# Kernel optimization log

Measured on AMD Instinct MI355X. Metric: run time of the kernel, lower is better.

The kernel has to match this reference:

```python
import jax, jax.numpy as jnp
import numpy as np

N = 50000       # nodes
E = 800000      # edges (avg degree 16)
IN = 256        # input feature dim
HID = 64        # per-head hidden dim
H = 2           # heads
C = 64          # num_classes (final single-head layer width)
NEG_SLOPE = 0.01  # torch F.leaky_relu default


def setup_inputs() -> dict:
    key = jax.random.key(0)
    ks = jax.random.split(key, 24)
    nrm = lambda k, shape, scale: jax.random.normal(k, shape, jnp.float32) * scale
    features = nrm(ks[0], (N, IN), 1.0)
    src = jax.random.randint(ks[1], (E,), 0, N)
    dst = jax.random.randint(ks[2], (E,), 0, N)
    # layer 0: H heads, Linear(IN->HID) + attn_l/attn_r Linear(HID->1)
    W0 = nrm(ks[3], (H, IN, HID), IN ** -0.5)
    b0 = jnp.zeros((H, HID), jnp.float32)
    al0 = nrm(ks[4], (H, HID), HID ** -0.5)
    bl0 = jnp.zeros((H,), jnp.float32)
    ar0 = nrm(ks[5], (H, HID), HID ** -0.5)
    br0 = jnp.zeros((H,), jnp.float32)
    # layer 1: H heads, Linear(H*HID->HID)
    W1 = nrm(ks[6], (H, H * HID, HID), (H * HID) ** -0.5)
    b1 = jnp.zeros((H, HID), jnp.float32)
    al1 = nrm(ks[7], (H, HID), HID ** -0.5)
    bl1 = jnp.zeros((H,), jnp.float32)
    ar1 = nrm(ks[8], (H, HID), HID ** -0.5)
    br1 = jnp.zeros((H,), jnp.float32)
    # final: 1 head, Linear(H*HID->C)
    Wf = nrm(ks[9], (1, H * HID, C), (H * HID) ** -0.5)
    bf = jnp.zeros((1, C), jnp.float32)
    alf = nrm(ks[10], (1, C), C ** -0.5)
    blf = jnp.zeros((1,), jnp.float32)
    arf = nrm(ks[11], (1, C), C ** -0.5)
    brf = jnp.zeros((1,), jnp.float32)
    return dict(features=features, src=src, dst=dst,
                W0=W0, b0=b0, al0=al0, bl0=bl0, ar0=ar0, br0=br0,
                W1=W1, b1=b1, al1=al1, bl1=bl1, ar1=ar1, br1=br1,
                Wf=Wf, bf=bf, alf=alf, blf=blf, arf=arf, brf=brf)


def gat_layer(x, src, dst, W, b, al, bl, ar, br):
    # x: [N, D]; W: [H, D, K]
    ft = jnp.einsum('nd,hdk->nhk', x, W) + b          # [N,H,K]
    a1 = jnp.einsum('nhk,hk->nh', ft, al) + bl        # [N,H] (dst-side)
    a2 = jnp.einsum('nhk,hk->nh', ft, ar) + br        # [N,H] (src-side)
    s = jax.nn.leaky_relu(a1[dst] + a2[src], NEG_SLOPE)  # [E,H]
    m = jax.ops.segment_max(s, dst, num_segments=N)      # per-dst max for stable softmax
    e = jnp.exp(s - m[dst])
    denom = jax.ops.segment_sum(e, dst, num_segments=N)
    alpha = e / denom[dst]                               # edge softmax over in-neighbors
    accum = jax.ops.segment_sum(alpha[:, :, None] * ft[src], dst, num_segments=N)  # [N,H,K]
    return jax.nn.elu(accum)


def reference(features, src, dst,
              W0, b0, al0, bl0, ar0, br0,
              W1, b1, al1, bl1, ar1, br1,
              Wf, bf, alf, blf, arf, brf):
    x = gat_layer(features, src, dst, W0, b0, al0, bl0, ar0, br0).reshape(N, H * HID)
    x = gat_layer(x, src, dst, W1, b1, al1, bl1, ar1, br1).reshape(N, H * HID)
    out = gat_layer(x, src, dst, Wf, bf, alf, blf, arf, brf)[:, 0, :]  # [N,C]
    return out
```

## Files before the change

kernel.cpp:

```cpp
#include <hip/hip_runtime.h>
#include <math.h>

#define NN 50000
#define EE 800000
#define DIN 256
#define NEG_SLOPE 0.01f

typedef __attribute__((ext_vector_type(8))) short bf16x8;
typedef __attribute__((ext_vector_type(8))) unsigned short u16x8;
typedef __attribute__((ext_vector_type(4))) float f32x4;
typedef __attribute__((ext_vector_type(2))) _Float16 f16x2;

__device__ __forceinline__ unsigned short bf16_rne(float f) {
    unsigned int u = __float_as_uint(f);
    u += 0x7fffu + ((u >> 16) & 1u);
    return (unsigned short)(u >> 16);
}
__device__ __forceinline__ float bf16_tof(unsigned short h) {
    return __uint_as_float(((unsigned int)h) << 16);
}

__global__ __launch_bounds__(256) void histrank_kernel(const int* __restrict__ dst,
                                                       int* __restrict__ cnt,
                                                       int* __restrict__ pos, int E) {
    int e = blockIdx.x * 256 + threadIdx.x;
    if (e < E) pos[e] = atomicAdd(&cnt[dst[e]], 1);
}

__global__ __launch_bounds__(1024) void scanA_kernel(const int* __restrict__ cnt,
                                                     int* __restrict__ off,
                                                     int* __restrict__ aux, int Nn) {
    __shared__ int wsums[16];
    int tid = threadIdx.x, lane = tid & 63, w = tid >> 6;
    int i = blockIdx.x * 1024 + tid;
    int v = (i < Nn) ? cnt[i] : 0;
    int x = v;
#pragma unroll
    for (int d = 1; d < 64; d <<= 1) {
        int y = __shfl_up(x, d);
        if (lane >= d) x += y;
    }
    if (lane == 63) wsums[w] = x;
    __syncthreads();
    if (w == 0 && lane < 16) {
        int ws = wsums[lane];
#pragma unroll
        for (int d = 1; d < 16; d <<= 1) {
            int y = __shfl_up(ws, d);
            if (lane >= d) ws += y;
        }
        wsums[lane] = ws;
    }
    __syncthreads();
    int incl = x + (w > 0 ? wsums[w - 1] : 0);
    if (i < Nn) off[i + 1] = incl;
    if (tid == 1023) aux[blockIdx.x] = incl;
}

__global__ __launch_bounds__(1024) void scanC_kernel(const int* __restrict__ aux,
                                                     int* __restrict__ off, int Nn) {
    int b = blockIdx.x;
    int prefix = 0;
    for (int j = 0; j < b; j++) prefix += aux[j];
    int i = b * 1024 + threadIdx.x;
    if (i < Nn) off[i + 1] += prefix;
    if (i == 0 && b == 0) off[0] = 0;
}

__global__ __launch_bounds__(256) void scatter_kernel(const int* __restrict__ src,
                                                      const int* __restrict__ dst,
                                                      const int* __restrict__ off,
                                                      const int* __restrict__ pos,
                                                      int* __restrict__ esrc, int E) {
    int e = blockIdx.x * 256 + threadIdx.x;
    if (e >= E) return;
    int d = dst[e];
    esrc[off[d] + pos[e]] = src[e];
}

__global__ __launch_bounds__(256) void conv_w_kernel(
    const float* __restrict__ W0, const float* __restrict__ W1,
    const float* __restrict__ Wf, unsigned short* __restrict__ w0h,
    unsigned short* __restrict__ w0l, unsigned short* __restrict__ w1h,
    unsigned short* __restrict__ w1l, unsigned short* __restrict__ wfh,
    unsigned short* __restrict__ wfl) {
    int t = blockIdx.x * 256 + threadIdx.x;
    const float* W;
    unsigned short *oh, *ol;
    int D, u;
    if (t < 32768) { W = W0; oh = w0h; ol = w0l; D = 256; u = t; }
    else if (t < 49152) { W = W1; oh = w1h; ol = w1l; D = 128; u = t - 32768; }
    else if (t < 57344) { W = Wf; oh = wfh; ol = wfl; D = 128; u = t - 49152; }
    else return;
    int d = u & (D - 1);
    int n = u / D;
    float v = W[((size_t)(n >> 6) * D + d) * 64 + (n & 63)];
    unsigned short hi = bf16_rne(v);
    unsigned short lo = bf16_rne(v - bf16_tof(hi));
    oh[(size_t)n * D + d] = hi;
    ol[(size_t)n * D + d] = lo;
}

#define LDK 40

template <int NCOL, bool AFP32>
__global__ __launch_bounds__(256) void gemm_attn(
    const float* __restrict__ Xf, const unsigned short* __restrict__ Xhi,
    const unsigned short* __restrict__ Xlo, const unsigned short* __restrict__ Wthi,
    const unsigned short* __restrict__ Wtlo, const float* __restrict__ bias,
    const float* __restrict__ al, const float* __restrict__ bl,
    const float* __restrict__ ar, const float* __restrict__ br,
    _Float16* __restrict__ FT, float* __restrict__ A1, float* __restrict__ A2,
    int Nn, int D) {
    const int H = NCOL / 64;
    const int NC16 = NCOL / 16;
    __shared__ __align__(16) unsigned short Ahi_s[64 * LDK];
    __shared__ __align__(16) unsigned short Alo_s[64 * LDK];
    __shared__ __align__(16) unsigned short Bhi_s[NCOL * LDK];
    __shared__ __align__(16) unsigned short Blo_s[NCOL * LDK];

    int tid = threadIdx.x;
    int wv = tid >> 6, l = tid & 63, lm = l & 15, quad = l >> 4;
    int m0 = blockIdx.x * 64;

    f32x4 acc[NC16];
#pragma unroll
    for (int c = 0; c < NC16; c++) acc[c] = (f32x4){0.f, 0.f, 0.f, 0.f};

    for (int d0 = 0; d0 < D; d0 += 32) {
        if (AFP32) {
#pragma unroll
            for (int i = 0; i < 2; i++) {
                int u = tid + i * 256;
                int row = u >> 3, c4 = u & 7;
                float4 v = make_float4(0.f, 0.f, 0.f, 0.f);
                if (m0 + row < Nn)
                    v = *(const float4*)&Xf[(size_t)(m0 + row) * D + d0 + c4 * 4];
                float f[4] = {v.x, v.y, v.z, v.w};
                unsigned short hi[4], lo[4];
#pragma unroll
                for (int j = 0; j < 4; j++) {
                    hi[j] = bf16_rne(f[j]);
                    lo[j] = bf16_rne(f[j] - bf16_tof(hi[j]));
                }
                *(ushort4*)&Ahi_s[row * LDK + c4 * 4] = make_ushort4(hi[0], hi[1], hi[2], hi[3]);
                *(ushort4*)&Alo_s[row * LDK + c4 * 4] = make_ushort4(lo[0], lo[1], lo[2], lo[3]);
            }
        } else {
            int row = tid >> 2, q = tid & 3;
            u16x8 vh = (u16x8)0, vl = (u16x8)0;
            if (m0 + row < Nn) {
                vh = *(const u16x8*)&Xhi[(size_t)(m0 + row) * D + d0 + q * 8];
                vl = *(const u16x8*)&Xlo[(size_t)(m0 + row) * D + d0 + q * 8];
            }
            *(u16x8*)&Ahi_s[row * LDK + q * 8] = vh;
            *(u16x8*)&Alo_s[row * LDK + q * 8] = vl;
        }
#pragma unroll
        for (int i = 0; i < NCOL / 64; i++) {
            int u = tid + i * 256;
            int n = u >> 2, q = u & 3;
            *(u16x8*)&Bhi_s[n * LDK + q * 8] =
                *(const u16x8*)&Wthi[(size_t)n * D + d0 + q * 8];
            *(u16x8*)&Blo_s[n * LDK + q * 8] =
                *(const u16x8*)&Wtlo[(size_t)n * D + d0 + q * 8];
        }
        __syncthreads();

        int arow = wv * 16 + lm;
        bf16x8 ah = *(const bf16x8*)&Ahi_s[arow * LDK + quad * 8];
        bf16x8 alo = *(const bf16x8*)&Alo_s[arow * LDK + quad * 8];
#pragma unroll
        for (int c = 0; c < NC16; c++) {
            bf16x8 bh = *(const bf16x8*)&Bhi_s[(c * 16 + lm) * LDK + quad * 8];
            bf16x8 blo = *(const bf16x8*)&Blo_s[(c * 16 + lm) * LDK + quad * 8];
            acc[c] = __builtin_amdgcn_mfma_f32_16x16x32_bf16(ah, bh, acc[c], 0, 0, 0);
            acc[c] = __builtin_amdgcn_mfma_f32_16x16x32_bf16(ah, blo, acc[c], 0, 0, 0);
            acc[c] = __builtin_amdgcn_mfma_f32_16x16x32_bf16(alo, bh, acc[c], 0, 0, 0);
        }
        __syncthreads();
    }

    float bj[NC16], alj[NC16], arj[NC16];
#pragma unroll
    for (int c = 0; c < NC16; c++) {
        bj[c] = bias[c * 16 + lm];
        alj[c] = al[c * 16 + lm];
        arj[c] = ar[c * 16 + lm];
    }
#pragma unroll
    for (int reg = 0; reg < 4; reg++) {
        int row = m0 + wv * 16 + quad * 4 + reg;
        bool ok = row < Nn;
        float s1[H], s2[H];
#pragma unroll
        for (int h = 0; h < H; h++) { s1[h] = 0.f; s2[h] = 0.f; }
#pragma unroll
        for (int c = 0; c < NC16; c++) {
            float o = acc[c][reg] + bj[c];
            int h = c >> 2;
            s1[h] += o * alj[c];
            s2[h] += o * arj[c];
            if (ok) FT[(size_t)row * NCOL + c * 16 + lm] = (_Float16)o;
        }
#pragma unroll
        for (int h = 0; h < H; h++) {
#pragma unroll
            for (int d = 1; d < 16; d <<= 1) {
                s1[h] += __shfl_xor(s1[h], d);
                s2[h] += __shfl_xor(s2[h], d);
            }
        }
        if (ok && lm == 0) {
#pragma unroll
            for (int h = 0; h < H; h++) {
                A1[(size_t)row * H + h] = s1[h] + bl[h];
                A2[(size_t)row * H + h] = s2[h] + br[h];
            }
        }
    }
}

__global__ __launch_bounds__(256) void agg2_kernel(
    const _Float16* __restrict__ ft, const float* __restrict__ a1,
    const float* __restrict__ a2, const int* __restrict__ off,
    const int* __restrict__ esrc, unsigned short* __restrict__ ohi,
    unsigned short* __restrict__ olo, int Nn) {
    __shared__ __align__(16) float ws[4][128];
    __shared__ __align__(16) int sjs[4][64];
    int wv = threadIdx.x >> 6, lane = threadIdx.x & 63;
    int n = blockIdx.x * 4 + wv;
    if (n >= Nn) return;
    int o0 = off[n], deg = off[n + 1] - o0;
    int hs = lane >> 5, cl2 = lane * 2;
    if (deg == 0) {
        *(ushort2*)&ohi[(size_t)n * 128 + cl2] = make_ushort2(0, 0);
        *(ushort2*)&olo[(size_t)n * 128 + cl2] = make_ushort2(0, 0);
        return;
    }
    float2 a1v = *(const float2*)&a1[(size_t)n * 2];
    float ax = 0.f, ay = 0.f;
    float ds0 = 0.f, ds1 = 0.f;
    for (int e0 = 0; e0 < deg; e0 += 64) {
        int nE = min(64, deg - e0);
        float w0 = 0.f, w1 = 0.f;
        int sj = 0;
        if (lane < nE) {
            sj = esrc[o0 + e0 + lane];
            float2 a2j = *(const float2*)&a2[(size_t)sj * 2];
            float t0 = a1v.x + a2j.x;
            float t1 = a1v.y + a2j.y;
            t0 = t0 > 0.f ? t0 : NEG_SLOPE * t0;
            t1 = t1 > 0.f ? t1 : NEG_SLOPE * t1;
            w0 = __expf(t0);
            w1 = __expf(t1);
        }
        ds0 += w0;
        ds1 += w1;
        *(float2*)&ws[wv][lane * 2] = make_float2(w0, w1);
        sjs[wv][lane] = sj;
        int j = 0;
        for (; j + 8 <= nE; j += 8) {
            float wb[8];
            int sb[8];
#pragma unroll
            for (int u = 0; u < 8; u++) {
                wb[u] = ws[wv][(j + u) * 2 + hs];
                sb[u] = sjs[wv][j + u];
            }
            f16x2 f[8];
#pragma unroll
            for (int u = 0; u < 8; u++)
                f[u] = *(const f16x2*)&ft[(size_t)sb[u] * 128 + cl2];
#pragma unroll
            for (int u = 0; u < 8; u++) {
                ax += wb[u] * (float)f[u].x;
                ay += wb[u] * (float)f[u].y;
            }
        }
        for (; j < nE; j++) {
            float w = ws[wv][j * 2 + hs];
            int s0 = sjs[wv][j];
            f16x2 f = *(const f16x2*)&ft[(size_t)s0 * 128 + cl2];
            ax += w * (float)f.x;
            ay += w * (float)f.y;
        }
    }
#pragma unroll
    for (int d = 1; d < 64; d <<= 1) {
        ds0 += __shfl_xor(ds0, d);
        ds1 += __shfl_xor(ds1, d);
    }
    float rd = 1.f / (hs ? ds1 : ds0);
    float rx = ax * rd, ry = ay * rd;
    rx = rx > 0.f ? rx : expm1f(rx);
    ry = ry > 0.f ? ry : expm1f(ry);
    unsigned short hx = bf16_rne(rx), hy = bf16_rne(ry);
    unsigned short lx = bf16_rne(rx - bf16_tof(hx)), ly = bf16_rne(ry - bf16_tof(hy));
    *(ushort2*)&ohi[(size_t)n * 128 + cl2] = make_ushort2(hx, hy);
    *(ushort2*)&olo[(size_t)n * 128 + cl2] = make_ushort2(lx, ly);
}

__global__ __launch_bounds__(256) void agg1_kernel(
    const _Float16* __restrict__ ft, const float* __restrict__ a1,
    const float* __restrict__ a2, const int* __restrict__ off,
    const int* __restrict__ esrc, float* __restrict__ out, int Nn) {
    __shared__ __align__(16) float ws[4][64];
    __shared__ __align__(16) int sjs[4][64];
    int wv = threadIdx.x >> 6, lane = threadIdx.x & 63;
    int n = blockIdx.x * 4 + wv;
    if (n >= Nn) return;
    int o0 = off[n], deg = off[n + 1] - o0;
    if (deg == 0) {
        out[(size_t)n * 64 + lane] = 0.f;
        return;
    }
    float a1v = a1[n];
    float acc = 0.f, dsum = 0.f;
    for (int e0 = 0; e0 < deg; e0 += 64) {
        int nE = min(64, deg - e0);
        float wl = 0.f;
        int sj = 0;
        if (lane < nE) {
            sj = esrc[o0 + e0 + lane];
            float t = a1v + a2[sj];
            t = t > 0.f ? t : NEG_SLOPE * t;
            wl = __expf(t);
        }
        dsum += wl;
        ws[wv][lane] = wl;
        sjs[wv][lane] = sj;
        int j = 0;
        for (; j + 8 <= nE; j += 8) {
            float wb[8];
            int sb[8];
#pragma unroll
            for (int u = 0; u < 8; u++) {
                wb[u] = ws[wv][j + u];
                sb[u] = sjs[wv][j + u];
            }
            _Float16 f[8];
#pragma unroll
            for (int u = 0; u < 8; u++) f[u] = ft[(size_t)sb[u] * 64 + lane];
#pragma unroll
            for (int u = 0; u < 8; u++) acc += wb[u] * (float)f[u];
        }
        for (; j < nE; j++)
            acc += ws[wv][j] * (float)ft[(size_t)sjs[wv][j] * 64 + lane];
    }
#pragma unroll
    for (int d = 1; d < 64; d <<= 1) dsum += __shfl_xor(dsum, d);
    float r = acc / dsum;
    out[(size_t)n * 64 + lane] = r > 0.f ? r : expm1f(r);
}

extern "C" void kernel_launch(void* const* d_in, const int* in_sizes, int n_in,
                              void* d_out, int out_size, void* d_ws, size_t ws_size,
                              hipStream_t stream) {
    const float* features = (const float*)d_in[0];
    const int* src = (const int*)d_in[1];
    const int* dst = (const int*)d_in[2];
    const float* W0 = (const float*)d_in[3];
    const float* b0 = (const float*)d_in[4];
    const float* al0 = (const float*)d_in[5];
    const float* bl0 = (const float*)d_in[6];
    const float* ar0 = (const float*)d_in[7];
    const float* br0 = (const float*)d_in[8];
    const float* W1 = (const float*)d_in[9];
    const float* b1 = (const float*)d_in[10];
    const float* al1 = (const float*)d_in[11];
    const float* bl1 = (const float*)d_in[12];
    const float* ar1 = (const float*)d_in[13];
    const float* br1 = (const float*)d_in[14];
    const float* Wf = (const float*)d_in[15];
    const float* bf = (const float*)d_in[16];
    const float* alf = (const float*)d_in[17];
    const float* blf = (const float*)d_in[18];
    const float* arf = (const float*)d_in[19];
    const float* brf = (const float*)d_in[20];

    char* p = (char*)d_ws;
    auto carve = [&](size_t bytes) {
        void* q = (void*)p;
        p += (bytes + 255) & ~(size_t)255;
        return q;
    };
    _Float16* ft = (_Float16*)carve((size_t)NN * 128 * 2);
    unsigned short* Xhi = (unsigned short*)carve((size_t)NN * 128 * 2);
    unsigned short* Xlo = (unsigned short*)carve((size_t)NN * 128 * 2);
    float* a1 = (float*)carve((size_t)NN * 2 * 4);
    float* a2 = (float*)carve((size_t)NN * 2 * 4);
    int* off = (int*)carve((size_t)(NN + 1) * 4);
    int* cnt = (int*)carve((size_t)NN * 4);
    int* esrc = (int*)carve((size_t)EE * 4);
    int* pos = (int*)carve((size_t)EE * 4);
    int* aux = (int*)carve(64 * 4);
    unsigned short* w0h = (unsigned short*)carve(32768 * 2);
    unsigned short* w0l = (unsigned short*)carve(32768 * 2);
    unsigned short* w1h = (unsigned short*)carve(16384 * 2);
    unsigned short* w1l = (unsigned short*)carve(16384 * 2);
    unsigned short* wfh = (unsigned short*)carve(8192 * 2);
    unsigned short* wfl = (unsigned short*)carve(8192 * 2);

    const int NB_SCAN = (NN + 1023) / 1024;
    const int GE = (EE + 255) / 256;

    hipMemsetAsync(cnt, 0, (size_t)NN * 4, stream);
    histrank_kernel<<<GE, 256, 0, stream>>>(dst, cnt, pos, EE);
    scanA_kernel<<<NB_SCAN, 1024, 0, stream>>>(cnt, off, aux, NN);
    scanC_kernel<<<NB_SCAN, 1024, 0, stream>>>(aux, off, NN);
    scatter_kernel<<<GE, 256, 0, stream>>>(src, dst, off, pos, esrc, EE);
    conv_w_kernel<<<(57344 + 255) / 256, 256, 0, stream>>>(W0, W1, Wf, w0h, w0l, w1h,
                                                           w1l, wfh, wfl);

    const int gx = (NN + 63) / 64;
    const int gn = (NN + 3) / 4;

    gemm_attn<128, true><<<gx, 256, 0, stream>>>(features, nullptr, nullptr, w0h, w0l,
                                                 b0, al0, bl0, ar0, br0, ft, a1, a2,
                                                 NN, DIN);
    agg2_kernel<<<gn, 256, 0, stream>>>(ft, a1, a2, off, esrc, Xhi, Xlo, NN);

    gemm_attn<128, false><<<gx, 256, 0, stream>>>(nullptr, Xhi, Xlo, w1h, w1l, b1, al1,
                                                  bl1, ar1, br1, ft, a1, a2, NN, 128);
    agg2_kernel<<<gn, 256, 0, stream>>>(ft, a1, a2, off, esrc, Xhi, Xlo, NN);

    gemm_attn<64, false><<<gx, 256, 0, stream>>>(nullptr, Xhi, Xlo, wfh, wfl, bf, alf,
                                                 blf, arf, brf, ft, a1, a2, NN, 128);
    agg1_kernel<<<gn, 256, 0, stream>>>(ft, a1, a2, off, esrc, (float*)d_out, NN);
}
```

Measured before the change: 339.4 us.

## Vectorize GAT aggregation gathers to 16-byte loads with cross-lane reduction

Both aggregation kernels now give each lane 8 contiguous fp16 features, read with one 16-byte load. Instead of every lane walking all edges for its own 1-2 columns, a wavefront handles several edges at once (4 edge groups in agg2, 8 in agg1), and the partial sums are combined with xor shuffles at the end. This cuts the number of gather instructions and widens each memory transaction, aiming at the gather-bound edge loop. The cost is a shuffle reduction over 8 accumulators, extra registers, and wasted work on tail edges when the degree is not a multiple of the group size.

```diff
diff --git a/kernel.cpp b/kernel.cpp
--- a/kernel.cpp
+++ b/kernel.cpp
@@ -9,7 +9,7 @@
 typedef __attribute__((ext_vector_type(8))) short bf16x8;
 typedef __attribute__((ext_vector_type(8))) unsigned short u16x8;
 typedef __attribute__((ext_vector_type(4))) float f32x4;
-typedef __attribute__((ext_vector_type(2))) _Float16 f16x2;
+typedef __attribute__((ext_vector_type(8))) _Float16 f16x8;
 
 __device__ __forceinline__ unsigned short bf16_rne(float f) {
     unsigned int u = __float_as_uint(f);
@@ -232,15 +232,21 @@
     int n = blockIdx.x * 4 + wv;
     if (n >= Nn) return;
     int o0 = off[n], deg = off[n + 1] - o0;
-    int hs = lane >> 5, cl2 = lane * 2;
+    int eg = lane >> 4, c = lane & 15, head = c >> 3;
     if (deg == 0) {
-        *(ushort2*)&ohi[(size_t)n * 128 + cl2] = make_ushort2(0, 0);
-        *(ushort2*)&olo[(size_t)n * 128 + cl2] = make_ushort2(0, 0);
+        if (lane < 16) {
+            u16x8 z = (u16x8)0;
+            *(u16x8*)&ohi[(size_t)n * 128 + c * 8] = z;
+            *(u16x8*)&olo[(size_t)n * 128 + c * 8] = z;
+        }
         return;
     }
     float2 a1v = *(const float2*)&a1[(size_t)n * 2];
-    float ax = 0.f, ay = 0.f;
+    float acc8[8];
+#pragma unroll
+    for (int k = 0; k < 8; k++) acc8[k] = 0.f;
     float ds0 = 0.f, ds1 = 0.f;
+
     for (int e0 = 0; e0 < deg; e0 += 64) {
         int nE = min(64, deg - e0);
         float w0 = 0.f, w1 = 0.f;
@@ -259,31 +265,14 @@
         ds1 += w1;
         *(float2*)&ws[wv][lane * 2] = make_float2(w0, w1);
         sjs[wv][lane] = sj;
-        int j = 0;
-        for (; j + 8 <= nE; j += 8) {
-            float wb[8];
-            int sb[8];
-#pragma unroll
-            for (int u = 0; u < 8; u++) {
-                wb[u] = ws[wv][(j + u) * 2 + hs];
-                sb[u] = sjs[wv][j + u];
-            }
-            f16x2 f[8];
-#pragma unroll
-            for (int u = 0; u < 8; u++)
-                f[u] = *(const f16x2*)&ft[(size_t)sb[u] * 128 + cl2];
-#pragma unroll
-            for (int u = 0; u < 8; u++) {
-                ax += wb[u] * (float)f[u].x;
-                ay += wb[u] * (float)f[u].y;
-            }
-        }
-        for (; j < nE; j++) {
-            float w = ws[wv][j * 2 + hs];
-            int s0 = sjs[wv][j];
-            f16x2 f = *(const f16x2*)&ft[(size_t)s0 * 128 + cl2];
-            ax += w * (float)f.x;
-            ay += w * (float)f.y;
+#pragma unroll 4
+        for (int j = 0; j < nE; j += 4) {
+            int jj = j + eg;
+            float w = (jj < nE) ? ws[wv][jj * 2 + head] : 0.f;
+            int s0 = sjs[wv][jj & 63];
+            f16x8 f = *(const f16x8*)&ft[(size_t)s0 * 128 + c * 8];
+#pragma unroll
+            for (int k = 0; k < 8; k++) acc8[k] += w * (float)f[k];
         }
     }
 #pragma unroll
@@ -291,14 +280,25 @@
         ds0 += __shfl_xor(ds0, d);
         ds1 += __shfl_xor(ds1, d);
     }
-    float rd = 1.f / (hs ? ds1 : ds0);
-    float rx = ax * rd, ry = ay * rd;
-    rx = rx > 0.f ? rx : expm1f(rx);
-    ry = ry > 0.f ? ry : expm1f(ry);
-    unsigned short hx = bf16_rne(rx), hy = bf16_rne(ry);
-    unsigned short lx = bf16_rne(rx - bf16_tof(hx)), ly = bf16_rne(ry - bf16_tof(hy));
-    *(ushort2*)&ohi[(size_t)n * 128 + cl2] = make_ushort2(hx, hy);
-    *(ushort2*)&olo[(size_t)n * 128 + cl2] = make_ushort2(lx, ly);
+#pragma unroll
+    for (int k = 0; k < 8; k++) {
+        acc8[k] += __shfl_xor(acc8[k], 16);
+        acc8[k] += __shfl_xor(acc8[k], 32);
+    }
+    if (lane < 16) {
+        float rd = 1.f / (head ? ds1 : ds0);
+        u16x8 hi8, lo8;
+#pragma unroll
+        for (int k = 0; k < 8; k++) {
+            float r = acc8[k] * rd;
+            r = r > 0.f ? r : expm1f(r);
+            unsigned short h = bf16_rne(r);
+            hi8[k] = h;
+            lo8[k] = bf16_rne(r - bf16_tof(h));
+        }
+        *(u16x8*)&ohi[(size_t)n * 128 + c * 8] = hi8;
+        *(u16x8*)&olo[(size_t)n * 128 + c * 8] = lo8;
+    }
 }
 
 __global__ __launch_bounds__(256) void agg1_kernel(
@@ -311,12 +311,19 @@
     int n = blockIdx.x * 4 + wv;
     if (n >= Nn) return;
     int o0 = off[n], deg = off[n + 1] - o0;
+    int eg = lane >> 3, c = lane & 7;
     if (deg == 0) {
-        out[(size_t)n * 64 + lane] = 0.f;
+        if (lane < 8) {
+            *(float4*)&out[(size_t)n * 64 + c * 8] = make_float4(0, 0, 0, 0);
+            *(float4*)&out[(size_t)n * 64 + c * 8 + 4] = make_float4(0, 0, 0, 0);
+        }
         return;
     }
     float a1v = a1[n];
-    float acc = 0.f, dsum = 0.f;
+    float acc8[8];
+#pragma unroll
+    for (int k = 0; k < 8; k++) acc8[k] = 0.f;
+    float dsum = 0.f;
     for (int e0 = 0; e0 < deg; e0 += 64) {
         int nE = min(64, deg - e0);
         float wl = 0.f;
@@ -330,28 +337,35 @@
         dsum += wl;
         ws[wv][lane] = wl;
         sjs[wv][lane] = sj;
-        int j = 0;
-        for (; j + 8 <= nE; j += 8) {
-            float wb[8];
-            int sb[8];
-#pragma unroll
-            for (int u = 0; u < 8; u++) {
-                wb[u] = ws[wv][j + u];
-                sb[u] = sjs[wv][j + u];
-            }
-            _Float16 f[8];
-#pragma unroll
-            for (int u = 0; u < 8; u++) f[u] = ft[(size_t)sb[u] * 64 + lane];
-#pragma unroll
-            for (int u = 0; u < 8; u++) acc += wb[u] * (float)f[u];
-        }
-        for (; j < nE; j++)
-            acc += ws[wv][j] * (float)ft[(size_t)sjs[wv][j] * 64 + lane];
+#pragma unroll 4
+        for (int j = 0; j < nE; j += 8) {
+            int jj = j + eg;
+            float w = (jj < nE) ? ws[wv][jj] : 0.f;
+            int s0 = sjs[wv][jj & 63];
+            f16x8 f = *(const f16x8*)&ft[(size_t)s0 * 64 + c * 8];
+#pragma unroll
+            for (int k = 0; k < 8; k++) acc8[k] += w * (float)f[k];
+        }
     }
 #pragma unroll
     for (int d = 1; d < 64; d <<= 1) dsum += __shfl_xor(dsum, d);
-    float r = acc / dsum;
-    out[(size_t)n * 64 + lane] = r > 0.f ? r : expm1f(r);
+#pragma unroll
+    for (int k = 0; k < 8; k++) {
+        acc8[k] += __shfl_xor(acc8[k], 8);
+        acc8[k] += __shfl_xor(acc8[k], 16);
+        acc8[k] += __shfl_xor(acc8[k], 32);
+    }
+    if (lane < 8) {
+        float rd = 1.f / dsum;
+        float r[8];
+#pragma unroll
+        for (int k = 0; k < 8; k++) {
+            r[k] = acc8[k] * rd;
+            r[k] = r[k] > 0.f ? r[k] : expm1f(r[k]);
+        }
+        *(float4*)&out[(size_t)n * 64 + c * 8] = make_float4(r[0], r[1], r[2], r[3]);
+        *(float4*)&out[(size_t)n * 64 + c * 8 + 4] = make_float4(r[4], r[5], r[6], r[7]);
+    }
 }
 
 extern "C" void kernel_launch(void* const* d_in, const int* in_sizes, int n_in,
```

Result: slower. 346.2 us (+2.0%).

## Merge preprocessing launches: fuse histogram with weight conversion, scatter with first GEMM

Applied to the files above, without the earlier changes.

Cuts the launch count by combining independent work into shared grids. The histogram/rank pass and the weight bf16 split run in one kernel. The two-pass scan becomes a single kernel where each block recomputes its prefix from the counts. The CSR scatter shares a grid with the layer-0 GEMM, so their blocks can overlap. This trades launch gaps and serialization for redundant prefix reads in later scan blocks and a larger mixed-role grid.

```diff
diff --git a/kernel.cpp b/kernel.cpp
--- a/kernel.cpp
+++ b/kernel.cpp
@@ -20,71 +20,20 @@
     return __uint_as_float(((unsigned int)h) << 16);
 }
 
-__global__ __launch_bounds__(256) void histrank_kernel(const int* __restrict__ dst,
-                                                       int* __restrict__ cnt,
-                                                       int* __restrict__ pos, int E) {
-    int e = blockIdx.x * 256 + threadIdx.x;
-    if (e < E) pos[e] = atomicAdd(&cnt[dst[e]], 1);
-}
-
-__global__ __launch_bounds__(1024) void scanA_kernel(const int* __restrict__ cnt,
-                                                     int* __restrict__ off,
-                                                     int* __restrict__ aux, int Nn) {
-    __shared__ int wsums[16];
-    int tid = threadIdx.x, lane = tid & 63, w = tid >> 6;
-    int i = blockIdx.x * 1024 + tid;
-    int v = (i < Nn) ? cnt[i] : 0;
-    int x = v;
-#pragma unroll
-    for (int d = 1; d < 64; d <<= 1) {
-        int y = __shfl_up(x, d);
-        if (lane >= d) x += y;
-    }
-    if (lane == 63) wsums[w] = x;
-    __syncthreads();
-    if (w == 0 && lane < 16) {
-        int ws = wsums[lane];
-#pragma unroll
-        for (int d = 1; d < 16; d <<= 1) {
-            int y = __shfl_up(ws, d);
-            if (lane >= d) ws += y;
-        }
-        wsums[lane] = ws;
-    }
-    __syncthreads();
-    int incl = x + (w > 0 ? wsums[w - 1] : 0);
-    if (i < Nn) off[i + 1] = incl;
-    if (tid == 1023) aux[blockIdx.x] = incl;
-}
-
-__global__ __launch_bounds__(1024) void scanC_kernel(const int* __restrict__ aux,
-                                                     int* __restrict__ off, int Nn) {
-    int b = blockIdx.x;
-    int prefix = 0;
-    for (int j = 0; j < b; j++) prefix += aux[j];
-    int i = b * 1024 + threadIdx.x;
-    if (i < Nn) off[i + 1] += prefix;
-    if (i == 0 && b == 0) off[0] = 0;
-}
-
-__global__ __launch_bounds__(256) void scatter_kernel(const int* __restrict__ src,
-                                                      const int* __restrict__ dst,
-                                                      const int* __restrict__ off,
-                                                      const int* __restrict__ pos,
-                                                      int* __restrict__ esrc, int E) {
-    int e = blockIdx.x * 256 + threadIdx.x;
-    if (e >= E) return;
-    int d = dst[e];
-    esrc[off[d] + pos[e]] = src[e];
-}
-
-__global__ __launch_bounds__(256) void conv_w_kernel(
+__global__ __launch_bounds__(256) void fused_pre(
+    const int* __restrict__ dst, int* __restrict__ cnt, int* __restrict__ pos, int E,
     const float* __restrict__ W0, const float* __restrict__ W1,
     const float* __restrict__ Wf, unsigned short* __restrict__ w0h,
     unsigned short* __restrict__ w0l, unsigned short* __restrict__ w1h,
     unsigned short* __restrict__ w1l, unsigned short* __restrict__ wfh,
-    unsigned short* __restrict__ wfl) {
-    int t = blockIdx.x * 256 + threadIdx.x;
+    unsigned short* __restrict__ wfl, int histBlocks) {
+    int b = blockIdx.x;
+    if (b < histBlocks) {
+        int e = b * 256 + threadIdx.x;
+        if (e < E) pos[e] = atomicAdd(&cnt[dst[e]], 1);
+        return;
+    }
+    int t = (b - histBlocks) * 256 + threadIdx.x;
     const float* W;
     unsigned short *oh, *ol;
     int D, u;
@@ -101,11 +50,59 @@
     ol[(size_t)n * D + d] = lo;
 }
 
+__global__ __launch_bounds__(1024) void scan_one(const int* __restrict__ cnt,
+                                                 int* __restrict__ off, int Nn) {
+    __shared__ int wsums[16];
+    __shared__ int s_prefix;
+    int tid = threadIdx.x, lane = tid & 63, w = tid >> 6;
+    int base = blockIdx.x * 1024;
+    int p = 0;
+    for (int i = tid; i < base; i += 1024) p += cnt[i];
+#pragma unroll
+    for (int d = 1; d < 64; d <<= 1) p += __shfl_xor(p, d);
+    if (tid < 16) wsums[tid] = 0;
+    __syncthreads();
+    if (lane == 0) wsums[w] = p;
+    __syncthreads();
+    if (tid == 0) {
+        int t = 0;
+#pragma unroll
+        for (int k = 0; k < 16; k++) t += wsums[k];
+        s_prefix = t;
+    }
+    __syncthreads();
+    int prefix = s_prefix;
+    __syncthreads();
+    int i = base + tid;
+    int v = (i < Nn) ? cnt[i] : 0;
+    int x = v;
+#pragma unroll
+    for (int d = 1; d < 64; d <<= 1) {
+        int y = __shfl_up(x, d);
+        if (lane >= d) x += y;
+    }
+    if (lane == 63) wsums[w] = x;
+    __syncthreads();
+    if (w == 0 && lane < 16) {
+        int ws = wsums[lane];
+#pragma unroll
+        for (int d = 1; d < 16; d <<= 1) {
+            int y = __shfl_up(ws, d);
+            if (lane >= d) ws += y;
+        }
+        wsums[lane] = ws;
+    }
+    __syncthreads();
+    int incl = x + (w > 0 ? wsums[w - 1] : 0);
+    if (i < Nn) off[i + 1] = prefix + incl;
+    if (blockIdx.x == 0 && tid == 0) off[0] = 0;
+}
+
 #define LDK 40
 
 template <int NCOL, bool AFP32>
-__global__ __launch_bounds__(256) void gemm_attn(
-    const float* __restrict__ Xf, const unsigned short* __restrict__ Xhi,
+__device__ __forceinline__ void gemm_body(
+    int bx, const float* __restrict__ Xf, const unsigned short* __restrict__ Xhi,
     const unsigned short* __restrict__ Xlo, const unsigned short* __restrict__ Wthi,
     const unsigned short* __restrict__ Wtlo, const float* __restrict__ bias,
     const float* __restrict__ al, const float* __restrict__ bl,
@@ -121,7 +118,7 @@
 
     int tid = threadIdx.x;
     int wv = tid >> 6, l = tid & 63, lm = l & 15, quad = l >> 4;
-    int m0 = blockIdx.x * 64;
+    int m0 = bx * 64;
 
     f32x4 acc[NC16];
 #pragma unroll
@@ -219,6 +216,40 @@
             }
         }
     }
+}
+
+template <int NCOL, bool AFP32>
+__global__ __launch_bounds__(256) void gemm_attn(
+    const float* __restrict__ Xf, const unsigned short* __restrict__ Xhi,
+    const unsigned short* __restrict__ Xlo, const unsigned short* __restrict__ Wthi,
+    const unsigned short* __restrict__ Wtlo, const float* __restrict__ bias,
+    const float* __restrict__ al, const float* __restrict__ bl,
+    const float* __restrict__ ar, const float* __restrict__ br,
+    _Float16* __restrict__ FT, float* __restrict__ A1, float* __restrict__ A2,
+    int Nn, int D) {
+    gemm_body<NCOL, AFP32>(blockIdx.x, Xf, Xhi, Xlo, Wthi, Wtlo, bias, al, bl, ar, br,
+                           FT, A1, A2, Nn, D);
+}
+
+__global__ __launch_bounds__(256) void fused_mid(
+    const int* __restrict__ src, const int* __restrict__ dst,
+    const int* __restrict__ off, const int* __restrict__ pos,
+    int* __restrict__ esrc, int E, const float* __restrict__ Xf,
+    const unsigned short* __restrict__ Wthi, const unsigned short* __restrict__ Wtlo,
+    const float* __restrict__ bias, const float* __restrict__ al,
+    const float* __restrict__ bl, const float* __restrict__ ar,
+    const float* __restrict__ br, _Float16* __restrict__ FT,
+    float* __restrict__ A1, float* __restrict__ A2, int Nn, int D, int scBlocks) {
+    if (blockIdx.x < scBlocks) {
+        int e = blockIdx.x * 256 + threadIdx.x;
+        if (e < E) {
+            int d = dst[e];
+            esrc[off[d] + pos[e]] = src[e];
+        }
+        return;
+    }
+    gemm_body<128, true>(blockIdx.x - scBlocks, Xf, nullptr, nullptr, Wthi, Wtlo,
+                         bias, al, bl, ar, br, FT, A1, A2, Nn, D);
 }
 
 __global__ __launch_bounds__(256) void agg2_kernel(
@@ -394,7 +425,6 @@
     int* cnt = (int*)carve((size_t)NN * 4);
     int* esrc = (int*)carve((size_t)EE * 4);
     int* pos = (int*)carve((size_t)EE * 4);
-    int* aux = (int*)carve(64 * 4);
     unsigned short* w0h = (unsigned short*)carve(32768 * 2);
     unsigned short* w0l = (unsigned short*)carve(32768 * 2);
     unsigned short* w1h = (unsigned short*)carve(16384 * 2);
@@ -404,27 +434,21 @@
 
     const int NB_SCAN = (NN + 1023) / 1024;
     const int GE = (EE + 255) / 256;
-
-    hipMemsetAsync(cnt, 0, (size_t)NN * 4, stream);
-    histrank_kernel<<<GE, 256, 0, stream>>>(dst, cnt, pos, EE);
-    scanA_kernel<<<NB_SCAN, 1024, 0, stream>>>(cnt, off, aux, NN);
-    scanC_kernel<<<NB_SCAN, 1024, 0, stream>>>(aux, off, NN);
-    scatter_kernel<<<GE, 256, 0, stream>>>(src, dst, off, pos, esrc, EE);
-    conv_w_kernel<<<(57344 + 255) / 256, 256, 0, stream>>>(W0, W1, Wf, w0h, w0l, w1h,
-                                                           w1l, wfh, wfl);
-
+    const int CONVB = (57344 + 255) / 256;
     const int gx = (NN + 63) / 64;
     const int gn = (NN + 3) / 4;
 
-    gemm_attn<128, true><<<gx, 256, 0, stream>>>(features, nullptr, nullptr, w0h, w0l,
-                                                 b0, al0, bl0, ar0, br0, ft, a1, a2,
-                                                 NN, DIN);
+    hipMemsetAsync(cnt, 0, (size_t)NN * 4, stream);
+    fused_pre<<<GE + CONVB, 256, 0, stream>>>(dst, cnt, pos, EE, W0, W1, Wf, w0h, w0l,
+                                              w1h, w1l, wfh, wfl, GE);
+    scan_one<<<NB_SCAN, 1024, 0, stream>>>(cnt, off, NN);
+    fused_mid<<<GE + gx, 256, 0, stream>>>(src, dst, off, pos, esrc, EE, features,
+                                           w0h, w0l, b0, al0, bl0, ar0, br0, ft, a1,
+                                           a2, NN, DIN, GE);
     agg2_kernel<<<gn, 256, 0, stream>>>(ft, a1, a2, off, esrc, Xhi, Xlo, NN);
-
     gemm_attn<128, false><<<gx, 256, 0, stream>>>(nullptr, Xhi, Xlo, w1h, w1l, b1, al1,
                                                   bl1, ar1, br1, ft, a1, a2, NN, 128);
     agg2_kernel<<<gn, 256, 0, stream>>>(ft, a1, a2, off, esrc, Xhi, Xlo, NN);
-
     gemm_attn<64, false><<<gx, 256, 0, stream>>>(nullptr, Xhi, Xlo, wfh, wfl, bf, alf,
                                                  blf, arf, brf, ft, a1, a2, NN, 128);
     agg1_kernel<<<gn, 256, 0, stream>>>(ft, a1, a2, off, esrc, (float*)d_out, NN);
```

Result: no change. 340.0 us (+0.2%).
